# Performance work log

Hardware: AMD Instinct MI355X
Metric: run time of the kernel (lower is better)

## Reference

```python
import jax, jax.numpy as jnp
import numpy as np
import math

# ----- sizes -----
NUM_EDGES = 16384
NUM_NODES = 1024          # senders index into [0, NUM_NODES)
N_MUL = 64                # multiplicity n = V.shape[1]
AVG_NEIGH = 16.0          # avg_num_neighbors
F_IN = 64                 # scalar feature dim of x

# ----- real spherical harmonics (component normalization: sum_m Y_lm^2 = 2l+1) -----
_S3 = math.sqrt(3.0); _S5 = math.sqrt(5.0); _S15 = math.sqrt(15.0)
_C33 = math.sqrt(70.0)/4.0; _C32 = math.sqrt(105.0)/2.0
_C31 = math.sqrt(42.0)/4.0; _C30 = math.sqrt(7.0)/2.0; _CXYZ = math.sqrt(105.0)

def _sph(vn):
    x, y, z = vn[:, 0], vn[:, 1], vn[:, 2]
    Y0 = jnp.ones_like(x)[:, None]
    Y1 = _S3 * vn
    Y2 = jnp.stack([_S15*x*y, _S15*y*z, 0.5*_S5*(3*z*z - 1), _S15*x*z, 0.5*_S15*(x*x - y*y)], axis=1)
    Y3 = jnp.stack([_C33*y*(3*x*x - y*y), _CXYZ*x*y*z, _C31*y*(5*z*z - 1), _C30*z*(5*z*z - 3), _C31*x*(5*z*z - 1), _C32*z*(x*x - y*y), _C33*x*(x*x - 3*y*y)], axis=1)
    return [Y0, Y1, Y2, Y3]

# monomial form of the same SH, used to derive EXACT Clebsch-Gordan coefficients
_SHP = {
    0: [[(1.0, (0,0,0))]],
    1: [[(_S3, (1,0,0))], [(_S3, (0,1,0))], [(_S3, (0,0,1))]],
    2: [[(_S15, (1,1,0))], [(_S15, (0,1,1))], [(1.5*_S5, (0,0,2)), (-0.5*_S5, (0,0,0))], [(_S15, (1,0,1))], [(0.5*_S15, (2,0,0)), (-0.5*_S15, (0,2,0))]],
    3: [[(3*_C33, (2,1,0)), (-_C33, (0,3,0))], [(_CXYZ, (1,1,1))], [(5*_C31, (0,1,2)), (-_C31, (0,1,0))], [(5*_C30, (0,0,3)), (-3*_C30, (0,0,1))], [(5*_C31, (1,0,2)), (-_C31, (1,0,0))], [(_C32, (2,0,1)), (-_C32, (0,2,1))], [(_C33, (3,0,0)), (-3*_C33, (1,2,0))]],
}

def _dfact(n):
    r = 1
    while n > 1:
        r *= n; n -= 2
    return r

def _mono_int(e):
    # exact integral of x^a y^b z^c over the unit sphere
    a, b, c = e
    if (a % 2) or (b % 2) or (c % 2):
        return 0.0
    return 4.0*math.pi*_dfact(a-1)*_dfact(b-1)*_dfact(c-1)/_dfact(a+b+c+1)

def _pmul(p, q):
    return [(cp*cq, (a1+a2, b1+b2, c1+c2)) for cp, (a1,b1,c1) in p for cq, (a2,b2,c2) in q]

def _pint(p):
    return sum(c*_mono_int(e) for c, e in p)

def _cg(l1, l2, l3):
    # unique SO(3) intertwiner in this real-SH basis, scaled like e3nn component norm: sqrt(2l3+1)*w3j
    C = np.zeros((2*l1+1, 2*l2+1, 2*l3+1))
    for i, p1 in enumerate(_SHP[l1]):
        for j, p2 in enumerate(_SHP[l2]):
            p12 = _pmul(p1, p2)
            for k, p3 in enumerate(_SHP[l3]):
                C[i, j, k] = _pint(_pmul(p12, p3)) / (4.0*math.pi)
    return jnp.asarray(C / np.linalg.norm(C) * np.sqrt(2*l3+1), dtype=jnp.float32)

# tensor-product paths surviving filter_ir_out = 0e + 1o + 2e (inputs: SH 0e+1o+2e+3o, V 0e+1o+2e)
_PATHS0 = [(0,0), (1,1), (2,2)]
_PATHS1 = [(0,1), (1,0), (1,2), (2,1), (3,2)]
_PATHS2 = [(0,2), (1,1), (2,0), (2,2), (3,1)]
CGS = {(l1, l2, l3): _cg(l1, l2, l3) for l3, ps in ((0, _PATHS0), (1, _PATHS1), (2, _PATHS2)) for l1, l2 in ps}

# e3nn normalize_function(silu): divide by sqrt(E_{z~N(0,1)}[silu(z)^2])
_zg = np.linspace(-12.0, 12.0, 200001)
_phi = np.exp(-0.5*_zg*_zg)/np.sqrt(2.0*np.pi)
_sl = _zg/(1.0 + np.exp(-_zg))
ACT_C = float(np.sqrt(np.sum(_sl*_sl*_phi)*(_zg[1]-_zg[0])))

def _nsilu(v):
    return jax.nn.silu(v) / ACT_C

def _forward(vectors, x, V, senders, W_w, W1, W2, W3, Wv1, Wv2):
    E, n = V.shape[0], V.shape[1]
    d = jnp.linalg.norm(vectors, axis=1, keepdims=True)                 # [E,1] edge lengths
    vn = vectors / d
    Y = jnp.concatenate(_sph(vn), axis=1)                               # [E,16], ell = 0..3
    w = (x @ W_w) / math.sqrt(x.shape[1])                               # [E,n] edge weights (1-layer MLP, no act)
    wY = w[:, :, None] * Y[:, None, :]                                  # [E,n,16]
    agg = jax.ops.segment_sum(wY, senders, num_segments=NUM_NODES)[senders]  # scatter_sum + map_back
    agg = agg / math.sqrt(AVG_NEIGH)
    A = jnp.split(agg, [1, 4, 9], axis=2)                               # SH chunks: dims 1,3,5,7
    B = jnp.split(V, [1, 4], axis=2)                                    # V chunks: dims 1,3,5
    def tp(l1, l2, l3):
        return jnp.einsum('eni,enj,ijk->enk', A[l1], B[l2], CGS[(l1, l2, l3)])
    scal = jnp.concatenate([tp(a, b, 0) for a, b in _PATHS0], axis=2)   # [E,n,3] new scalars
    V1 = jnp.concatenate([tp(a, b, 1) for a, b in _PATHS1], axis=1)     # [E,5n,3] 1o paths
    V2 = jnp.concatenate([tp(a, b, 2) for a, b in _PATHS2], axis=1)     # [E,5n,5] 2e paths
    h = jnp.concatenate([x, scal.reshape(E, 3*n)], axis=1)              # [E, F_IN+3n]
    h = _nsilu(h @ W1 / math.sqrt(h.shape[1]))
    h = _nsilu(h @ W2 / math.sqrt(W2.shape[0]))
    h = h @ W3 / math.sqrt(W3.shape[0])                                 # output_activation=False
    # poly_envelope(p-1=5, 2), p=6: 1 - 28 d^6 + 48 d^7 - 21 d^8 on [0,1), 0 outside
    u = 1.0 - 28.0*d**6 + 48.0*d**7 - 21.0*d**8
    x_out = jnp.where(d < 1.0, u, 0.0) * h                              # [E,64]
    o1 = jnp.einsum('emi,mo->eoi', V1, Wv1) / math.sqrt(V1.shape[1])    # Linear per irrep: [E,n,3]
    o2 = jnp.einsum('emi,mo->eoi', V2, Wv2) / math.sqrt(V2.shape[1])    # [E,n,5]
    # output 0e block has no input path -> zeros (e3nn Linear, no bias)
    V_out = jnp.concatenate([jnp.zeros((E, n, 1), x_out.dtype), o1, o2], axis=2)  # [E,n,9]
    return x_out, V_out

def setup_inputs():
    key = jax.random.key(0)
    ks = jax.random.split(key, 10)
    E = NUM_EDGES
    vectors = 0.35 * jax.random.normal(ks[0], (E, 3), jnp.float32)   # mostly inside cutoff radius 1
    x = jax.random.normal(ks[1], (E, F_IN), jnp.float32)
    V = jax.random.normal(ks[2], (E, N_MUL, 9), jnp.float32)
    senders = jax.random.randint(ks[3], (E,), 0, NUM_NODES, dtype=jnp.int32)
    W_w = jax.random.normal(ks[4], (F_IN, N_MUL), jnp.float32)
    W1 = jax.random.normal(ks[5], (F_IN + 3*N_MUL, 64), jnp.float32)
    W2 = jax.random.normal(ks[6], (64, 64), jnp.float32)
    W3 = jax.random.normal(ks[7], (64, 64), jnp.float32)
    Wv1 = jax.random.normal(ks[8], (5*N_MUL, N_MUL), jnp.float32)
    Wv2 = jax.random.normal(ks[9], (5*N_MUL, N_MUL), jnp.float32)
    return {"vectors": vectors, "x": x, "V": V, "senders": senders, "W_w": W_w, "W1": W1, "W2": W2, "W3": W3, "Wv1": Wv1, "Wv2": Wv2}

def reference(vectors, x, V, senders, W_w, W1, W2, W3, Wv1, Wv2):
    return _forward(vectors, x, V, senders, W_w, W1, W2, W3, Wv1, Wv2)
```

## Files before the change

kernel.cpp:

```cpp
#include <hip/hip_runtime.h>
#include <math.h>

#define NNODES 1024
#define EB 4

typedef __attribute__((ext_vector_type(8))) short short8;
typedef __attribute__((ext_vector_type(4))) float f32x4;

__device__ __forceinline__ unsigned short f2bf(float f) {
  union { float f; unsigned int u; } v; v.f = f;
  unsigned int r = v.u + 0x7fffu + ((v.u >> 16) & 1u);
  return (unsigned short)(r >> 16);
}

struct CGPack { float v[576]; };

static const double H_SHC[16][2] = {
  {1.0, 0.0},
  {1.7320508075688772, 0.0},
  {1.7320508075688772, 0.0},
  {1.7320508075688772, 0.0},
  {3.8729833462074170, 0.0},
  {3.8729833462074170, 0.0},
  {3.3541019662496844, -1.1180339887498949},
  {3.8729833462074170, 0.0},
  {1.9364916731037085, -1.9364916731037085},
  {6.2749501990055667, -2.0916500663351889},
  {10.246950765959598, 0.0},
  {8.1009258730098255, -1.6201851746019651},
  {6.6143782776614768, -3.9686269665968861},
  {8.1009258730098255, -1.6201851746019651},
  {5.1234753829797990, -5.1234753829797990},
  {2.0916500663351889, -6.2749501990055667},
};
static const int H_SHE[16][2] = {
  {0,0},{1,0},{16,0},{256,0},
  {17,0},{272,0},{512,0},{257,0},{2,32},
  {18,48},{273,0},{528,16},{768,256},{513,1},{258,288},{3,33}};
static const int H_PL1[13] = {0,1,2, 0,1,1,2,3, 0,1,2,2,3};
static const int H_PL2[13] = {0,1,2, 1,0,2,1,2, 2,1,0,2,1};
static const int H_PL3[13] = {0,0,0, 1,1,1,1,1, 2,2,2,2,2};
static const int H_PCG[13] = {0,1,10, 35,44,53,98,143, 248,273,318,343,468};

static double h_dfact(int n) { double r = 1.0; while (n > 1) { r *= n; n -= 2; } return r; }

struct HostConsts {
  CGPack pack;
  float inv_actc;
  HostConsts() {
    const int LOFF[4] = {0,1,4,9};
    for (int p = 0; p < 13; p++) {
      int l1 = H_PL1[p], l2 = H_PL2[p], l3 = H_PL3[p];
      int n1 = 2*l1+1, n2 = 2*l2+1, n3 = 2*l3+1, nent = n1*n2*n3;
      double vals[125], ss = 0.0;
      for (int t = 0; t < nent; t++) {
        int i = t / (n2*n3);
        int rem = t - i*(n2*n3);
        int j = rem / n3;
        int k = rem - j*n3;
        int lm1 = LOFF[l1]+i, lm2 = LOFF[l2]+j, lm3 = LOFF[l3]+k;
        double v = 0.0;
        for (int t1 = 0; t1 < 2; t1++)
        for (int t2 = 0; t2 < 2; t2++)
        for (int t3 = 0; t3 < 2; t3++) {
          double cc = H_SHC[lm1][t1]*H_SHC[lm2][t2]*H_SHC[lm3][t3];
          if (cc == 0.0) continue;
          int s = H_SHE[lm1][t1] + H_SHE[lm2][t2] + H_SHE[lm3][t3];
          int a = s & 15, b = (s >> 4) & 15, c = (s >> 8) & 15;
          if (!((a|b|c) & 1))
            v += cc * (h_dfact(a-1)*h_dfact(b-1)*h_dfact(c-1) / h_dfact(a+b+c+1));
        }
        vals[t] = v; ss += v*v;
      }
      double scale = sqrt((double)(2*l3+1)) / sqrt(ss);
      for (int t = 0; t < nent; t++) pack.v[H_PCG[p]+t] = (float)(vals[t]*scale*0.25);
    }
    pack.v[573] = pack.v[574] = pack.v[575] = 0.f;
    double s = 0.0, dz = 24.0/200000.0;
    for (int i = 0; i <= 200000; i++) {
      double z = -12.0 + dz*i;
      double ph = exp(-0.5*z*z) * 0.39894228040143267794;
      double sl = z / (1.0 + exp(-z));
      s += sl*sl*ph;
    }
    inv_actc = (float)(1.0 / sqrt(s*dz));
  }
};

__global__ __launch_bounds__(256) void k_pre(
    const int* __restrict__ senders, int* __restrict__ counts, int* __restrict__ elist,
    const float* __restrict__ x, const float* __restrict__ Ww,
    float* __restrict__ w_ws,
    const float* __restrict__ Wv1, const float* __restrict__ Wv2,
    const float* __restrict__ W1, const float* __restrict__ W2, const float* __restrict__ W3,
    unsigned short* __restrict__ wv1f, unsigned short* __restrict__ wv2f,
    unsigned short* __restrict__ w1f, unsigned short* __restrict__ w2f,
    unsigned short* __restrict__ w3f,
    float inv_actc, int E)
{
  const int t = threadIdx.x;
  const int bid = blockIdx.x;
  const int nsc = (E + 255) >> 8;

  if (bid < nsc) {
    int e = bid*256 + t;
    if (e < E) {
      int s = senders[e];
      int pos = atomicAdd(&counts[s], 1) & 63;
      elist[s*64 + pos] = e;
    }
    return;
  }

  if (bid < nsc + 32) {
    const int wid = t >> 6, lane = t & 63;
    const int g = (bid - nsc)*4 + wid;
    const float ia = inv_actc;
    const float s320 = 0.05590169943749474f;
    const float* src; unsigned short* dst; int nk, f; float sc;
    if (g < 40)       { src = Wv1; dst = wv1f; nk = 10; f = g;       sc = s320; }
    else if (g < 80)  { src = Wv2; dst = wv2f; nk = 10; f = g - 40;  sc = s320; }
    else if (g < 112) { src = W1;  dst = w1f;  nk = 8;  f = g - 80;  sc = 0.0625f; }
    else if (g < 120) { src = W2;  dst = w2f;  nk = 2;  f = g - 112; sc = 0.125f*ia; }
    else              { src = W3;  dst = w3f;  nk = 2;  f = g - 120; sc = 0.125f*ia; }
    int nt = f / nk;
    int ks = f - nt*nk;
    unsigned short us[8];
    #pragma unroll
    for (int j = 0; j < 8; j++) {
      float v = src[(ks*32 + (lane>>4)*8 + j)*64 + nt*16 + (lane & 15)];
      us[j] = f2bf(v * sc);
    }
    uint4 pk;
    pk.x = (unsigned)us[0] | ((unsigned)us[1] << 16);
    pk.y = (unsigned)us[2] | ((unsigned)us[3] << 16);
    pk.z = (unsigned)us[4] | ((unsigned)us[5] << 16);
    pk.w = (unsigned)us[6] | ((unsigned)us[7] << 16);
    *(uint4*)(dst + ((size_t)f*64 + lane)*8) = pk;
    return;
  }

  __shared__ float xsh[64*64];
  const int eb0 = (bid - nsc - 32) * 64;
  for (int q = t; q < 1024; q += 256)
    ((f32x4*)xsh)[q] = ((const f32x4*)(x + (size_t)eb0*64))[q];

  const int n = t & 63;
  float ww[64];
  #pragma unroll
  for (int f = 0; f < 64; f++) ww[f] = Ww[f*64 + n];
  __syncthreads();

  const int er0 = (t >> 6) * 16;
  #pragma unroll
  for (int i = 0; i < 16; i++) {
    int e = er0 + i;
    const f32x4* xr = (const f32x4*)(&xsh[e*64]);
    float a0 = 0.f, a1 = 0.f, a2 = 0.f, a3 = 0.f;
    #pragma unroll
    for (int fq = 0; fq < 16; fq += 4) {
      f32x4 x0 = xr[fq+0], x1 = xr[fq+1], x2 = xr[fq+2], x3 = xr[fq+3];
      a0 = fmaf(x0.x, ww[fq*4+0],  fmaf(x0.y, ww[fq*4+1],  fmaf(x0.z, ww[fq*4+2],  fmaf(x0.w, ww[fq*4+3],  a0))));
      a1 = fmaf(x1.x, ww[fq*4+4],  fmaf(x1.y, ww[fq*4+5],  fmaf(x1.z, ww[fq*4+6],  fmaf(x1.w, ww[fq*4+7],  a1))));
      a2 = fmaf(x2.x, ww[fq*4+8],  fmaf(x2.y, ww[fq*4+9],  fmaf(x2.z, ww[fq*4+10], fmaf(x2.w, ww[fq*4+11], a2))));
      a3 = fmaf(x3.x, ww[fq*4+12], fmaf(x3.y, ww[fq*4+13], fmaf(x3.z, ww[fq*4+14], fmaf(x3.w, ww[fq*4+15], a3))));
    }
    w_ws[(size_t)(eb0+e)*64 + n] = ((a0+a1)+(a2+a3)) * 0.125f;
  }
}

__global__ __launch_bounds__(256) void k_node(
    const float* __restrict__ vec, const float* __restrict__ w_ws,
    const int* __restrict__ counts, const int* __restrict__ elist,
    float* __restrict__ node_agg)
{
  __shared__ float red[4*1024];
  const int wid = threadIdx.x >> 6, lane = threadIdx.x & 63;
  const int s = blockIdx.x;
  const int deg = min(counts[s], 64);

  const float S3 = 1.7320508075688772f, S5 = 2.23606797749979f, S15 = 3.872983346207417f;
  const float C33 = 2.091650066335189f, C32 = 5.123475382979799f, C31 = 1.6201851746019651f;
  const float C30 = 1.3228756555322954f, CX = 10.246950765959598f;

  float A[16];
  #pragma unroll
  for (int k = 0; k < 16; k++) A[k] = 0.f;

  for (int ii = wid; ii < deg; ii += 4) {
    int e = elist[s*64 + ii];
    float wv = w_ws[(size_t)e*64 + lane];
    float vx = vec[e*3+0], vy = vec[e*3+1], vz = vec[e*3+2];
    float d = sqrtf(vx*vx + vy*vy + vz*vz);
    float X = vx/d, Yv = vy/d, Z = vz/d;
    float y[16];
    y[0] = 1.f;
    y[1] = S3*X;  y[2] = S3*Yv;  y[3] = S3*Z;
    y[4] = S15*X*Yv; y[5] = S15*Yv*Z; y[6] = 0.5f*S5*(3.f*Z*Z - 1.f);
    y[7] = S15*X*Z;  y[8] = 0.5f*S15*(X*X - Yv*Yv);
    y[9]  = C33*Yv*(3.f*X*X - Yv*Yv);
    y[10] = CX*X*Yv*Z;
    y[11] = C31*Yv*(5.f*Z*Z - 1.f);
    y[12] = C30*Z*(5.f*Z*Z - 3.f);
    y[13] = C31*X*(5.f*Z*Z - 1.f);
    y[14] = C32*Z*(X*X - 3.f*Yv*Yv)*0.f + C32*Z*(X*X - Yv*Yv);
    y[14] = C32*Z*(X*X - Yv*Yv);
    y[15] = C33*X*(X*X - 3.f*Yv*Yv);
    #pragma unroll
    for (int k = 0; k < 16; k++) A[k] = fmaf(wv, y[k], A[k]);
  }
  #pragma unroll
  for (int k = 0; k < 16; k++) red[wid*1024 + lane*16 + k] = A[k];
  __syncthreads();
  const int t = threadIdx.x;
  f32x4 v0 = ((f32x4*)red)[t];
  f32x4 v1 = ((f32x4*)red)[256 + t];
  f32x4 v2 = ((f32x4*)red)[512 + t];
  f32x4 v3 = ((f32x4*)red)[768 + t];
  f32x4 sum = v0 + v1 + v2 + v3;
  ((f32x4*)(node_agg + (size_t)s*1024))[t] = sum;
}

template<int L1, int L2, int L3>
__device__ __forceinline__ void tp_path(const float* __restrict__ cgp,
    const float a[16], const float b[9], float o[2*L3+1])
{
  constexpr int N1 = 2*L1+1, N2 = 2*L2+1, N3 = 2*L3+1;
  constexpr int AO = (L1==0) ? 0 : (L1==1) ? 1 : (L1==2) ? 4 : 9;
  constexpr int BO = (L2==0) ? 0 : (L2==1) ? 1 : 4;
  constexpr int LM1 = (L1==0) ? 0 : (L1==1) ? 1 : (L1==2) ? 4 : 9;
  constexpr int LM2 = (L2==0) ? 0 : (L2==1) ? 1 : 4;
  constexpr int LM3 = (L3==0) ? 0 : (L3==1) ? 1 : 4;
  static constexpr unsigned char PAR[16] =
      {0, 1,2,4, 3,6,0,5,0, 2,7,2,4,1,4,1};
  #pragma unroll
  for (int k = 0; k < N3; k++) o[k] = 0.f;
  int ci = 0;
  #pragma unroll
  for (int i = 0; i < N1; i++) {
    #pragma unroll
    for (int j = 0; j < N2; j++) {
      float ab = a[AO+i] * b[BO+j];
      #pragma unroll
      for (int k = 0; k < N3; k++) {
        if ((PAR[LM1+i] ^ PAR[LM2+j] ^ PAR[LM3+k]) == 0)
          o[k] = fmaf(ab, cgp[ci], o[k]);
        ci++;
      }
    }
  }
}

__global__ __launch_bounds__(256, 6) void edge_main(
    const float* __restrict__ vec, const float* __restrict__ x,
    const float* __restrict__ V, const int* __restrict__ senders,
    const float* __restrict__ node_agg, const CGPack P,
    const unsigned short* __restrict__ wv1f, const unsigned short* __restrict__ wv2f,
    const unsigned short* __restrict__ w1f, const unsigned short* __restrict__ w2f,
    const unsigned short* __restrict__ w3f,
    float* __restrict__ out, int E)
{
  __shared__ __align__(16) unsigned short V12sh[32*328];
  __shared__ __align__(16) unsigned short zrow[336];
  __shared__ __align__(16) unsigned short hsh[4*264];
  __shared__ __align__(16) unsigned short h1sh[4*72];
  __shared__ __align__(16) unsigned short h2sh[4*72];
  __shared__ __align__(16) float xosh[4*64];
  __shared__ float ush[EB];

  unsigned short* V1sh = V12sh;
  unsigned short* V2sh = V12sh + 12*328;
  float* vosh = (float*)V12sh;

  const float* cg = P.v;

  const int t = threadIdx.x;
  const int wid = t >> 6, lane = t & 63;
  const int e0 = blockIdx.x * EB;
  const size_t E64 = (size_t)E * 64;

  if (t < 168) ((unsigned int*)zrow)[t] = 0u;

  if (t < 64) {
    int el = t >> 4, off = (t & 15)*4;
    f32x4 xv = *(const f32x4*)(x + (size_t)(e0 + el)*64 + off);
    uint2 pk;
    pk.x = (unsigned)f2bf(xv.x) | ((unsigned)f2bf(xv.y) << 16);
    pk.y = (unsigned)f2bf(xv.z) | ((unsigned)f2bf(xv.w) << 16);
    *(uint2*)(hsh + el*264 + off) = pk;
  }

  {
    const int eloc = wid;
    const int eg = e0 + eloc;

    float b[9];
    const float* vp = V + (size_t)eg*576 + lane*9;
    #pragma unroll
    for (int j = 0; j < 9; j++) b[j] = vp[j];

    const int s = senders[eg];
    float a[16];
    const f32x4* nap = (const f32x4*)(node_agg + s*1024 + lane*16);
    #pragma unroll
    for (int q = 0; q < 4; q++) {
      f32x4 av = nap[q];
      a[q*4+0] = av.x; a[q*4+1] = av.y; a[q*4+2] = av.z; a[q*4+3] = av.w;
    }

    float o1[1], o3[3], o5[5];
    tp_path<0,0,0>(cg + 0,  a, b, o1); hsh[eloc*264 + 64 + lane*3 + 0] = f2bf(o1[0]);
    tp_path<1,1,0>(cg + 1,  a, b, o1); hsh[eloc*264 + 64 + lane*3 + 1] = f2bf(o1[0]);
    tp_path<2,2,0>(cg + 10, a, b, o1); hsh[eloc*264 + 64 + lane*3 + 2] = f2bf(o1[0]);
    tp_path<0,1,1>(cg + 35, a, b, o3);
    { int r = eloc*3; for (int i=0;i<3;i++) V1sh[(r+i)*328 + 0*64 + lane] = f2bf(o3[i]); }
    tp_path<1,0,1>(cg + 44, a, b, o3);
    { int r = eloc*3; for (int i=0;i<3;i++) V1sh[(r+i)*328 + 1*64 + lane] = f2bf(o3[i]); }
    tp_path<1,2,1>(cg + 53, a, b, o3);
    { int r = eloc*3; for (int i=0;i<3;i++) V1sh[(r+i)*328 + 2*64 + lane] = f2bf(o3[i]); }
    tp_path<2,1,1>(cg + 98, a, b, o3);
    { int r = eloc*3; for (int i=0;i<3;i++) V1sh[(r+i)*328 + 3*64 + lane] = f2bf(o3[i]); }
    tp_path<3,2,1>(cg + 143, a, b, o3);
    { int r = eloc*3; for (int i=0;i<3;i++) V1sh[(r+i)*328 + 4*64 + lane] = f2bf(o3[i]); }
    tp_path<0,2,2>(cg + 248, a, b, o5);
    { int r = eloc*5; for (int i=0;i<5;i++) V2sh[(r+i)*328 + 0*64 + lane] = f2bf(o5[i]); }
    tp_path<1,1,2>(cg + 273, a, b, o5);
    { int r = eloc*5; for (int i=0;i<5;i++) V2sh[(r+i)*328 + 1*64 + lane] = f2bf(o5[i]); }
    tp_path<2,0,2>(cg + 318, a, b, o5);
    { int r = eloc*5; for (int i=0;i<5;i++) V2sh[(r+i)*328 + 2*64 + lane] = f2bf(o5[i]); }
    tp_path<2,2,2>(cg + 343, a, b, o5);
    { int r = eloc*5; for (int i=0;i<5;i++) V2sh[(r+i)*328 + 3*64 + lane] = f2bf(o5[i]); }
    tp_path<3,1,2>(cg + 468, a, b, o5);
    { int r = eloc*5; for (int i=0;i<5;i++) V2sh[(r+i)*328 + 4*64 + lane] = f2bf(o5[i]); }

    if (lane == 0) {
      float vx = vec[eg*3+0], vy = vec[eg*3+1], vz = vec[eg*3+2];
      float d = sqrtf(vx*vx + vy*vy + vz*vz);
      float u = 0.f;
      if (d < 1.f) {
        float d3 = d*d*d, d6 = d3*d3, d7 = d6*d, d8 = d7*d;
        u = 1.f - 28.f*d6 + 48.f*d7 - 21.f*d8;
      }
      ush[eloc] = u;
    }
  }
  __syncthreads();

  const int ntile = wid;
  const int qr = lane >> 4;
  const int ml = lane & 15;

  f32x4 acc1 = (f32x4){0,0,0,0};
  {
    const unsigned short* p0 = (ml < 12) ? &V1sh[ml*328] : zrow;
    const unsigned short* bb = wv1f + ((size_t)(ntile*10)*64 + lane)*8;
    #pragma unroll
    for (int ks = 0; ks < 10; ks++) {
      short8 bf = *(const short8*)(bb + ks*512);
      short8 af = *(const short8*)(p0 + ks*32 + qr*8);
      acc1 = __builtin_amdgcn_mfma_f32_16x16x32_bf16(af, bf, acc1, 0, 0, 0);
    }
  }

  f32x4 acc2a = (f32x4){0,0,0,0}, acc2b = (f32x4){0,0,0,0};
  {
    const unsigned short* p0 = &V2sh[ml*328];
    const unsigned short* p1 = (16+ml < 20) ? &V2sh[(16+ml)*328] : zrow;
    const unsigned short* bb = wv2f + ((size_t)(ntile*10)*64 + lane)*8;
    #pragma unroll
    for (int ks = 0; ks < 10; ks++) {
      short8 bf = *(const short8*)(bb + ks*512);
      int ao = ks*32 + qr*8;
      short8 af0 = *(const short8*)(p0 + ao);
      short8 af1 = *(const short8*)(p1 + ao);
      acc2a = __builtin_amdgcn_mfma_f32_16x16x32_bf16(af0, bf, acc2a, 0, 0, 0);
      acc2b = __builtin_amdgcn_mfma_f32_16x16x32_bf16(af1, bf, acc2b, 0, 0, 0);
    }
  }

  const unsigned short* hp = (ml < 4) ? &hsh[ml*264] : zrow;
  {
    f32x4 c = (f32x4){0,0,0,0};
    const unsigned short* bb = w1f + ((size_t)(ntile*8)*64 + lane)*8;
    #pragma unroll
    for (int ks = 0; ks < 8; ks++) {
      short8 bf = *(const short8*)(bb + ks*512);
      short8 af = *(const short8*)(hp + ks*32 + qr*8);
      c = __builtin_amdgcn_mfma_f32_16x16x32_bf16(af, bf, c, 0, 0, 0);
    }
    #pragma unroll
    for (int r = 0; r < 4; r++) {
      int row = qr*4 + r;
      if (row < 4) {
        float v = c[r];
        float sv = v / (1.f + expf(-v));
        h1sh[row*72 + ntile*16 + ml] = f2bf(sv);
      }
    }
  }
  __syncthreads();

  #pragma unroll
  for (int r = 0; r < 4; r++) {
    int row = qr*4 + r;
    if (row < 12) {
      int el = row / 3, i = row - (row/3)*3;
      vosh[el*584 + (ntile*16+ml)*9 + 1 + i] = acc1[r];
    }
  }
  #pragma unroll
  for (int r = 0; r < 4; r++) {
    int row = qr*4 + r;
    int el = row / 5, i = row - (row/5)*5;
    vosh[el*584 + (ntile*16+ml)*9 + 4 + i] = acc2a[r];
  }
  #pragma unroll
  for (int r = 0; r < 4; r++) {
    int row = 16 + qr*4 + r;
    if (row < 20) {
      int el = row / 5, i = row - (row/5)*5;
      vosh[el*584 + (ntile*16+ml)*9 + 4 + i] = acc2b[r];
    }
  }
  { int el = t >> 6, o = t & 63;
    vosh[el*584 + o*9] = 0.f; }

  {
    f32x4 c = (f32x4){0,0,0,0};
    const unsigned short* ap = (ml < 4) ? &h1sh[ml*72] : zrow;
    const unsigned short* bb = w2f + ((size_t)(ntile*2)*64 + lane)*8;
    #pragma unroll
    for (int ks = 0; ks < 2; ks++) {
      short8 bf = *(const short8*)(bb + ks*512);
      short8 af = *(const short8*)(ap + ks*32 + qr*8);
      c = __builtin_amdgcn_mfma_f32_16x16x32_bf16(af, bf, c, 0, 0, 0);
    }
    #pragma unroll
    for (int r = 0; r < 4; r++) {
      int row = qr*4 + r;
      if (row < 4) {
        float v = c[r];
        float sv = v / (1.f + expf(-v));
        h2sh[row*72 + ntile*16 + ml] = f2bf(sv);
      }
    }
  }
  __syncthreads();

  {
    f32x4 c = (f32x4){0,0,0,0};
    const unsigned short* ap = (ml < 4) ? &h2sh[ml*72] : zrow;
    const unsigned short* bb = w3f + ((size_t)(ntile*2)*64 + lane)*8;
    #pragma unroll
    for (int ks = 0; ks < 2; ks++) {
      short8 bf = *(const short8*)(bb + ks*512);
      short8 af = *(const short8*)(ap + ks*32 + qr*8);
      c = __builtin_amdgcn_mfma_f32_16x16x32_bf16(af, bf, c, 0, 0, 0);
    }
    #pragma unroll
    for (int r = 0; r < 4; r++) {
      int row = qr*4 + r;
      if (row < 4) xosh[row*64 + ntile*16 + ml] = ush[row] * c[r];
    }
  }

  for (int q = t; q < 576; q += 256) {
    int el = q / 144, i4 = q - (q/144)*144;
    ((f32x4*)(out + E64 + (size_t)(e0+el)*576))[i4] = ((f32x4*)(vosh + el*584))[i4];
  }
  __syncthreads();

  if (t < 64)
    ((f32x4*)(out + (size_t)e0*64))[t] = ((f32x4*)xosh)[t];
}

extern "C" void kernel_launch(void* const* d_in, const int* in_sizes, int n_in,
                              void* d_out, int out_size, void* d_ws, size_t ws_size,
                              hipStream_t stream)
{
  const float* vec     = (const float*)d_in[0];
  const float* x       = (const float*)d_in[1];
  const float* V       = (const float*)d_in[2];
  const int*   senders = (const int*)  d_in[3];
  const float* Ww      = (const float*)d_in[4];
  const float* W1      = (const float*)d_in[5];
  const float* W2      = (const float*)d_in[6];
  const float* W3      = (const float*)d_in[7];
  const float* Wv1     = (const float*)d_in[8];
  const float* Wv2     = (const float*)d_in[9];
  float* out = (float*)d_out;
  const int E = in_sizes[0] / 3;

  static HostConsts HC;

  char* base = (char*)d_ws;
  float* node_agg = (float*)(base);
  float* w_ws     = (float*)(base + (4<<20));
  int* counts     = (int*)  (base + (8<<20) + 8192);
  int* elist      = (int*)  (base + (8<<20) + 12288);
  unsigned short* wv1f = (unsigned short*)(base + (8<<20) + 278528);
  unsigned short* wv2f = (unsigned short*)(base + (8<<20) + 319488);
  unsigned short* w1f  = (unsigned short*)(base + (8<<20) + 360448);
  unsigned short* w2f  = (unsigned short*)(base + (8<<20) + 393216);
  unsigned short* w3f  = (unsigned short*)(base + (8<<20) + 401408);

  hipMemsetAsync(counts, 0, NNODES*sizeof(int), stream);

  const int nsc = (E + 255) >> 8;
  const int ngemm = (E + 63) >> 6;
  k_pre<<<nsc + 32 + ngemm, 256, 0, stream>>>(senders, counts, elist,
                                      x, Ww, w_ws,
                                      Wv1, Wv2, W1, W2, W3,
                                      wv1f, wv2f, w1f, w2f, w3f, HC.inv_actc, E);
  k_node<<<NNODES, 256, 0, stream>>>(vec, w_ws, counts, elist, node_agg);
  edge_main<<<E/EB, 256, 0, stream>>>(vec, x, V, senders, node_agg, HC.pack,
                                      wv1f, wv2f, w1f, w2f, w3f, out, E);
}
```

Measured before the change: 165.9 us.

## Fuse three kernels into one persistent kernel with software grid barriers

```diff
diff --git a/kernel.cpp b/kernel.cpp
--- a/kernel.cpp
+++ b/kernel.cpp
@@ -3,6 +3,7 @@
 
 #define NNODES 1024
 #define EB 4
+#define GRID 1024
 
 typedef __attribute__((ext_vector_type(8))) short short8;
 typedef __attribute__((ext_vector_type(4))) float f32x4;
@@ -87,140 +88,6 @@
   }
 };
 
-__global__ __launch_bounds__(256) void k_pre(
-    const int* __restrict__ senders, int* __restrict__ counts, int* __restrict__ elist,
-    const float* __restrict__ x, const float* __restrict__ Ww,
-    float* __restrict__ w_ws,
-    const float* __restrict__ Wv1, const float* __restrict__ Wv2,
-    const float* __restrict__ W1, const float* __restrict__ W2, const float* __restrict__ W3,
-    unsigned short* __restrict__ wv1f, unsigned short* __restrict__ wv2f,
-    unsigned short* __restrict__ w1f, unsigned short* __restrict__ w2f,
-    unsigned short* __restrict__ w3f,
-    float inv_actc, int E)
-{
-  const int t = threadIdx.x;
-  const int bid = blockIdx.x;
-  const int nsc = (E + 255) >> 8;
-
-  if (bid < nsc) {
-    int e = bid*256 + t;
-    if (e < E) {
-      int s = senders[e];
-      int pos = atomicAdd(&counts[s], 1) & 63;
-      elist[s*64 + pos] = e;
-    }
-    return;
-  }
-
-  if (bid < nsc + 32) {
-    const int wid = t >> 6, lane = t & 63;
-    const int g = (bid - nsc)*4 + wid;
-    const float ia = inv_actc;
-    const float s320 = 0.05590169943749474f;
-    const float* src; unsigned short* dst; int nk, f; float sc;
-    if (g < 40)       { src = Wv1; dst = wv1f; nk = 10; f = g;       sc = s320; }
-    else if (g < 80)  { src = Wv2; dst = wv2f; nk = 10; f = g - 40;  sc = s320; }
-    else if (g < 112) { src = W1;  dst = w1f;  nk = 8;  f = g - 80;  sc = 0.0625f; }
-    else if (g < 120) { src = W2;  dst = w2f;  nk = 2;  f = g - 112; sc = 0.125f*ia; }
-    else              { src = W3;  dst = w3f;  nk = 2;  f = g - 120; sc = 0.125f*ia; }
-    int nt = f / nk;
-    int ks = f - nt*nk;
-    unsigned short us[8];
-    #pragma unroll
-    for (int j = 0; j < 8; j++) {
-      float v = src[(ks*32 + (lane>>4)*8 + j)*64 + nt*16 + (lane & 15)];
-      us[j] = f2bf(v * sc);
-    }
-    uint4 pk;
-    pk.x = (unsigned)us[0] | ((unsigned)us[1] << 16);
-    pk.y = (unsigned)us[2] | ((unsigned)us[3] << 16);
-    pk.z = (unsigned)us[4] | ((unsigned)us[5] << 16);
-    pk.w = (unsigned)us[6] | ((unsigned)us[7] << 16);
-    *(uint4*)(dst + ((size_t)f*64 + lane)*8) = pk;
-    return;
-  }
-
-  __shared__ float xsh[64*64];
-  const int eb0 = (bid - nsc - 32) * 64;
-  for (int q = t; q < 1024; q += 256)
-    ((f32x4*)xsh)[q] = ((const f32x4*)(x + (size_t)eb0*64))[q];
-
-  const int n = t & 63;
-  float ww[64];
-  #pragma unroll
-  for (int f = 0; f < 64; f++) ww[f] = Ww[f*64 + n];
-  __syncthreads();
-
-  const int er0 = (t >> 6) * 16;
-  #pragma unroll
-  for (int i = 0; i < 16; i++) {
-    int e = er0 + i;
-    const f32x4* xr = (const f32x4*)(&xsh[e*64]);
-    float a0 = 0.f, a1 = 0.f, a2 = 0.f, a3 = 0.f;
-    #pragma unroll
-    for (int fq = 0; fq < 16; fq += 4) {
-      f32x4 x0 = xr[fq+0], x1 = xr[fq+1], x2 = xr[fq+2], x3 = xr[fq+3];
-      a0 = fmaf(x0.x, ww[fq*4+0],  fmaf(x0.y, ww[fq*4+1],  fmaf(x0.z, ww[fq*4+2],  fmaf(x0.w, ww[fq*4+3],  a0))));
-      a1 = fmaf(x1.x, ww[fq*4+4],  fmaf(x1.y, ww[fq*4+5],  fmaf(x1.z, ww[fq*4+6],  fmaf(x1.w, ww[fq*4+7],  a1))));
-      a2 = fmaf(x2.x, ww[fq*4+8],  fmaf(x2.y, ww[fq*4+9],  fmaf(x2.z, ww[fq*4+10], fmaf(x2.w, ww[fq*4+11], a2))));
-      a3 = fmaf(x3.x, ww[fq*4+12], fmaf(x3.y, ww[fq*4+13], fmaf(x3.z, ww[fq*4+14], fmaf(x3.w, ww[fq*4+15], a3))));
-    }
-    w_ws[(size_t)(eb0+e)*64 + n] = ((a0+a1)+(a2+a3)) * 0.125f;
-  }
-}
-
-__global__ __launch_bounds__(256) void k_node(
-    const float* __restrict__ vec, const float* __restrict__ w_ws,
-    const int* __restrict__ counts, const int* __restrict__ elist,
-    float* __restrict__ node_agg)
-{
-  __shared__ float red[4*1024];
-  const int wid = threadIdx.x >> 6, lane = threadIdx.x & 63;
-  const int s = blockIdx.x;
-  const int deg = min(counts[s], 64);
-
-  const float S3 = 1.7320508075688772f, S5 = 2.23606797749979f, S15 = 3.872983346207417f;
-  const float C33 = 2.091650066335189f, C32 = 5.123475382979799f, C31 = 1.6201851746019651f;
-  const float C30 = 1.3228756555322954f, CX = 10.246950765959598f;
-
-  float A[16];
-  #pragma unroll
-  for (int k = 0; k < 16; k++) A[k] = 0.f;
-
-  for (int ii = wid; ii < deg; ii += 4) {
-    int e = elist[s*64 + ii];
-    float wv = w_ws[(size_t)e*64 + lane];
-    float vx = vec[e*3+0], vy = vec[e*3+1], vz = vec[e*3+2];
-    float d = sqrtf(vx*vx + vy*vy + vz*vz);
-    float X = vx/d, Yv = vy/d, Z = vz/d;
-    float y[16];
-    y[0] = 1.f;
-    y[1] = S3*X;  y[2] = S3*Yv;  y[3] = S3*Z;
-    y[4] = S15*X*Yv; y[5] = S15*Yv*Z; y[6] = 0.5f*S5*(3.f*Z*Z - 1.f);
-    y[7] = S15*X*Z;  y[8] = 0.5f*S15*(X*X - Yv*Yv);
-    y[9]  = C33*Yv*(3.f*X*X - Yv*Yv);
-    y[10] = CX*X*Yv*Z;
-    y[11] = C31*Yv*(5.f*Z*Z - 1.f);
-    y[12] = C30*Z*(5.f*Z*Z - 3.f);
-    y[13] = C31*X*(5.f*Z*Z - 1.f);
-    y[14] = C32*Z*(X*X - 3.f*Yv*Yv)*0.f + C32*Z*(X*X - Yv*Yv);
-    y[14] = C32*Z*(X*X - Yv*Yv);
-    y[15] = C33*X*(X*X - 3.f*Yv*Yv);
-    #pragma unroll
-    for (int k = 0; k < 16; k++) A[k] = fmaf(wv, y[k], A[k]);
-  }
-  #pragma unroll
-  for (int k = 0; k < 16; k++) red[wid*1024 + lane*16 + k] = A[k];
-  __syncthreads();
-  const int t = threadIdx.x;
-  f32x4 v0 = ((f32x4*)red)[t];
-  f32x4 v1 = ((f32x4*)red)[256 + t];
-  f32x4 v2 = ((f32x4*)red)[512 + t];
-  f32x4 v3 = ((f32x4*)red)[768 + t];
-  f32x4 sum = v0 + v1 + v2 + v3;
-  ((f32x4*)(node_agg + (size_t)s*1024))[t] = sum;
-}
-
 template<int L1, int L2, int L3>
 __device__ __forceinline__ void tp_path(const float* __restrict__ cgp,
     const float a[16], const float b[9], float o[2*L3+1])
@@ -251,13 +118,30 @@
   }
 }
 
-__global__ __launch_bounds__(256, 6) void edge_main(
+__device__ __forceinline__ void grid_bar(int* ctr, int nblk) {
+  __syncthreads();
+  if (threadIdx.x == 0) {
+    __threadfence();
+    __hip_atomic_fetch_add(ctr, 1, __ATOMIC_RELEASE, __HIP_MEMORY_SCOPE_AGENT);
+    while (__hip_atomic_load(ctr, __ATOMIC_ACQUIRE, __HIP_MEMORY_SCOPE_AGENT) < nblk)
+      __builtin_amdgcn_s_sleep(2);
+    __threadfence();
+  }
+  __syncthreads();
+}
+
+__global__ __launch_bounds__(256, 4) void mega(
     const float* __restrict__ vec, const float* __restrict__ x,
     const float* __restrict__ V, const int* __restrict__ senders,
-    const float* __restrict__ node_agg, const CGPack P,
-    const unsigned short* __restrict__ wv1f, const unsigned short* __restrict__ wv2f,
-    const unsigned short* __restrict__ w1f, const unsigned short* __restrict__ w2f,
-    const unsigned short* __restrict__ w3f,
+    const float* __restrict__ Ww,
+    const float* __restrict__ Wv1, const float* __restrict__ Wv2,
+    const float* __restrict__ W1, const float* __restrict__ W2, const float* __restrict__ W3,
+    const CGPack P, float inv_actc,
+    float* __restrict__ node_agg, float* __restrict__ w_ws,
+    int* __restrict__ counts, int* __restrict__ elist, int* __restrict__ bars,
+    unsigned short* __restrict__ wv1f, unsigned short* __restrict__ wv2f,
+    unsigned short* __restrict__ w1f, unsigned short* __restrict__ w2f,
+    unsigned short* __restrict__ w3f,
     float* __restrict__ out, int E)
 {
   __shared__ __align__(16) unsigned short V12sh[32*328];
@@ -268,210 +152,323 @@
   __shared__ __align__(16) float xosh[4*64];
   __shared__ float ush[EB];
 
+  const int t = threadIdx.x;
+  const int bid = blockIdx.x;
+  const int wid = t >> 6, lane = t & 63;
+  const int nblk = gridDim.x;
+
+  if (bid < 256) {
+    float* xsh = (float*)V12sh;
+    const int eb0 = bid * 64;
+    for (int q = t; q < 1024; q += 256)
+      ((f32x4*)xsh)[q] = ((const f32x4*)(x + (size_t)eb0*64))[q];
+    const int n = t & 63;
+    float ww[64];
+    #pragma unroll
+    for (int f = 0; f < 64; f++) ww[f] = Ww[f*64 + n];
+    __syncthreads();
+    const int er0 = (t >> 6) * 16;
+    #pragma unroll
+    for (int i = 0; i < 16; i++) {
+      int e = er0 + i;
+      const f32x4* xr = (const f32x4*)(&xsh[e*64]);
+      float a0 = 0.f, a1 = 0.f, a2 = 0.f, a3 = 0.f;
+      #pragma unroll
+      for (int fq = 0; fq < 16; fq += 4) {
+        f32x4 x0 = xr[fq+0], x1 = xr[fq+1], x2 = xr[fq+2], x3 = xr[fq+3];
+        a0 = fmaf(x0.x, ww[fq*4+0],  fmaf(x0.y, ww[fq*4+1],  fmaf(x0.z, ww[fq*4+2],  fmaf(x0.w, ww[fq*4+3],  a0))));
+        a1 = fmaf(x1.x, ww[fq*4+4],  fmaf(x1.y, ww[fq*4+5],  fmaf(x1.z, ww[fq*4+6],  fmaf(x1.w, ww[fq*4+7],  a1))));
+        a2 = fmaf(x2.x, ww[fq*4+8],  fmaf(x2.y, ww[fq*4+9],  fmaf(x2.z, ww[fq*4+10], fmaf(x2.w, ww[fq*4+11], a2))));
+        a3 = fmaf(x3.x, ww[fq*4+12], fmaf(x3.y, ww[fq*4+13], fmaf(x3.z, ww[fq*4+14], fmaf(x3.w, ww[fq*4+15], a3))));
+      }
+      w_ws[(size_t)(eb0+e)*64 + n] = ((a0+a1)+(a2+a3)) * 0.125f;
+    }
+  } else if (bid < 288) {
+    const int g = (bid - 256)*4 + wid;
+    const float ia = inv_actc;
+    const float s320 = 0.05590169943749474f;
+    const float* src; unsigned short* dst; int nk, f; float sc;
+    if (g < 40)       { src = Wv1; dst = wv1f; nk = 10; f = g;       sc = s320; }
+    else if (g < 80)  { src = Wv2; dst = wv2f; nk = 10; f = g - 40;  sc = s320; }
+    else if (g < 112) { src = W1;  dst = w1f;  nk = 8;  f = g - 80;  sc = 0.0625f; }
+    else if (g < 120) { src = W2;  dst = w2f;  nk = 2;  f = g - 112; sc = 0.125f*ia; }
+    else              { src = W3;  dst = w3f;  nk = 2;  f = g - 120; sc = 0.125f*ia; }
+    int nt = f / nk;
+    int ks = f - nt*nk;
+    unsigned short us[8];
+    #pragma unroll
+    for (int j = 0; j < 8; j++) {
+      float v = src[(ks*32 + (lane>>4)*8 + j)*64 + nt*16 + (lane & 15)];
+      us[j] = f2bf(v * sc);
+    }
+    uint4 pk;
+    pk.x = (unsigned)us[0] | ((unsigned)us[1] << 16);
+    pk.y = (unsigned)us[2] | ((unsigned)us[3] << 16);
+    pk.z = (unsigned)us[4] | ((unsigned)us[5] << 16);
+    pk.w = (unsigned)us[6] | ((unsigned)us[7] << 16);
+    *(uint4*)(dst + ((size_t)f*64 + lane)*8) = pk;
+  } else if (bid < 352) {
+    int e = (bid - 288)*256 + t;
+    if (e < E) {
+      int s = senders[e];
+      int pos = atomicAdd(&counts[s], 1) & 63;
+      elist[s*64 + pos] = e;
+    }
+  }
+
+  grid_bar(&bars[0], nblk);
+
+  {
+    float* red = (float*)V12sh;
+    const int s = bid;
+    const int deg = min(counts[s], 64);
+
+    const float S3 = 1.7320508075688772f, S5 = 2.23606797749979f, S15 = 3.872983346207417f;
+    const float C33 = 2.091650066335189f, C32 = 5.123475382979799f, C31 = 1.6201851746019651f;
+    const float C30 = 1.3228756555322954f, CX = 10.246950765959598f;
+
+    float A[16];
+    #pragma unroll
+    for (int k = 0; k < 16; k++) A[k] = 0.f;
+
+    for (int ii = wid; ii < deg; ii += 4) {
+      int e = elist[s*64 + ii];
+      float wv = w_ws[(size_t)e*64 + lane];
+      float vx = vec[e*3+0], vy = vec[e*3+1], vz = vec[e*3+2];
+      float d = sqrtf(vx*vx + vy*vy + vz*vz);
+      float X = vx/d, Yv = vy/d, Z = vz/d;
+      float y[16];
+      y[0] = 1.f;
+      y[1] = S3*X;  y[2] = S3*Yv;  y[3] = S3*Z;
+      y[4] = S15*X*Yv; y[5] = S15*Yv*Z; y[6] = 0.5f*S5*(3.f*Z*Z - 1.f);
+      y[7] = S15*X*Z;  y[8] = 0.5f*S15*(X*X - Yv*Yv);
+      y[9]  = C33*Yv*(3.f*X*X - Yv*Yv);
+      y[10] = CX*X*Yv*Z;
+      y[11] = C31*Yv*(5.f*Z*Z - 1.f);
+      y[12] = C30*Z*(5.f*Z*Z - 3.f);
+      y[13] = C31*X*(5.f*Z*Z - 1.f);
+      y[14] = C32*Z*(X*X - Yv*Yv);
+      y[15] = C33*X*(X*X - 3.f*Yv*Yv);
+      #pragma unroll
+      for (int k = 0; k < 16; k++) A[k] = fmaf(wv, y[k], A[k]);
+    }
+    #pragma unroll
+    for (int k = 0; k < 16; k++) red[wid*1024 + lane*16 + k] = A[k];
+    __syncthreads();
+    f32x4 v0 = ((f32x4*)red)[t];
+    f32x4 v1 = ((f32x4*)red)[256 + t];
+    f32x4 v2 = ((f32x4*)red)[512 + t];
+    f32x4 v3 = ((f32x4*)red)[768 + t];
+    f32x4 sum = v0 + v1 + v2 + v3;
+    ((f32x4*)(node_agg + (size_t)s*1024))[t] = sum;
+  }
+
+  grid_bar(&bars[1], nblk);
+
   unsigned short* V1sh = V12sh;
   unsigned short* V2sh = V12sh + 12*328;
   float* vosh = (float*)V12sh;
-
   const float* cg = P.v;
-
-  const int t = threadIdx.x;
-  const int wid = t >> 6, lane = t & 63;
-  const int e0 = blockIdx.x * EB;
   const size_t E64 = (size_t)E * 64;
-
-  if (t < 168) ((unsigned int*)zrow)[t] = 0u;
-
-  if (t < 64) {
-    int el = t >> 4, off = (t & 15)*4;
-    f32x4 xv = *(const f32x4*)(x + (size_t)(e0 + el)*64 + off);
-    uint2 pk;
-    pk.x = (unsigned)f2bf(xv.x) | ((unsigned)f2bf(xv.y) << 16);
-    pk.y = (unsigned)f2bf(xv.z) | ((unsigned)f2bf(xv.w) << 16);
-    *(uint2*)(hsh + el*264 + off) = pk;
-  }
-
-  {
-    const int eloc = wid;
-    const int eg = e0 + eloc;
-
-    float b[9];
-    const float* vp = V + (size_t)eg*576 + lane*9;
-    #pragma unroll
-    for (int j = 0; j < 9; j++) b[j] = vp[j];
-
-    const int s = senders[eg];
-    float a[16];
-    const f32x4* nap = (const f32x4*)(node_agg + s*1024 + lane*16);
-    #pragma unroll
-    for (int q = 0; q < 4; q++) {
-      f32x4 av = nap[q];
-      a[q*4+0] = av.x; a[q*4+1] = av.y; a[q*4+2] = av.z; a[q*4+3] = av.w;
-    }
-
-    float o1[1], o3[3], o5[5];
-    tp_path<0,0,0>(cg + 0,  a, b, o1); hsh[eloc*264 + 64 + lane*3 + 0] = f2bf(o1[0]);
-    tp_path<1,1,0>(cg + 1,  a, b, o1); hsh[eloc*264 + 64 + lane*3 + 1] = f2bf(o1[0]);
-    tp_path<2,2,0>(cg + 10, a, b, o1); hsh[eloc*264 + 64 + lane*3 + 2] = f2bf(o1[0]);
-    tp_path<0,1,1>(cg + 35, a, b, o3);
-    { int r = eloc*3; for (int i=0;i<3;i++) V1sh[(r+i)*328 + 0*64 + lane] = f2bf(o3[i]); }
-    tp_path<1,0,1>(cg + 44, a, b, o3);
-    { int r = eloc*3; for (int i=0;i<3;i++) V1sh[(r+i)*328 + 1*64 + lane] = f2bf(o3[i]); }
-    tp_path<1,2,1>(cg + 53, a, b, o3);
-    { int r = eloc*3; for (int i=0;i<3;i++) V1sh[(r+i)*328 + 2*64 + lane] = f2bf(o3[i]); }
-    tp_path<2,1,1>(cg + 98, a, b, o3);
-    { int r = eloc*3; for (int i=0;i<3;i++) V1sh[(r+i)*328 + 3*64 + lane] = f2bf(o3[i]); }
-    tp_path<3,2,1>(cg + 143, a, b, o3);
-    { int r = eloc*3; for (int i=0;i<3;i++) V1sh[(r+i)*328 + 4*64 + lane] = f2bf(o3[i]); }
-    tp_path<0,2,2>(cg + 248, a, b, o5);
-    { int r = eloc*5; for (int i=0;i<5;i++) V2sh[(r+i)*328 + 0*64 + lane] = f2bf(o5[i]); }
-    tp_path<1,1,2>(cg + 273, a, b, o5);
-    { int r = eloc*5; for (int i=0;i<5;i++) V2sh[(r+i)*328 + 1*64 + lane] = f2bf(o5[i]); }
-    tp_path<2,0,2>(cg + 318, a, b, o5);
-    { int r = eloc*5; for (int i=0;i<5;i++) V2sh[(r+i)*328 + 2*64 + lane] = f2bf(o5[i]); }
-    tp_path<2,2,2>(cg + 343, a, b, o5);
-    { int r = eloc*5; for (int i=0;i<5;i++) V2sh[(r+i)*328 + 3*64 + lane] = f2bf(o5[i]); }
-    tp_path<3,1,2>(cg + 468, a, b, o5);
-    { int r = eloc*5; for (int i=0;i<5;i++) V2sh[(r+i)*328 + 4*64 + lane] = f2bf(o5[i]); }
-
-    if (lane == 0) {
-      float vx = vec[eg*3+0], vy = vec[eg*3+1], vz = vec[eg*3+2];
-      float d = sqrtf(vx*vx + vy*vy + vz*vz);
-      float u = 0.f;
-      if (d < 1.f) {
-        float d3 = d*d*d, d6 = d3*d3, d7 = d6*d, d8 = d7*d;
-        u = 1.f - 28.f*d6 + 48.f*d7 - 21.f*d8;
-      }
-      ush[eloc] = u;
-    }
-  }
-  __syncthreads();
-
   const int ntile = wid;
   const int qr = lane >> 4;
   const int ml = lane & 15;
 
-  f32x4 acc1 = (f32x4){0,0,0,0};
-  {
-    const unsigned short* p0 = (ml < 12) ? &V1sh[ml*328] : zrow;
-    const unsigned short* bb = wv1f + ((size_t)(ntile*10)*64 + lane)*8;
-    #pragma unroll
-    for (int ks = 0; ks < 10; ks++) {
-      short8 bf = *(const short8*)(bb + ks*512);
-      short8 af = *(const short8*)(p0 + ks*32 + qr*8);
-      acc1 = __builtin_amdgcn_mfma_f32_16x16x32_bf16(af, bf, acc1, 0, 0, 0);
-    }
-  }
-
-  f32x4 acc2a = (f32x4){0,0,0,0}, acc2b = (f32x4){0,0,0,0};
-  {
-    const unsigned short* p0 = &V2sh[ml*328];
-    const unsigned short* p1 = (16+ml < 20) ? &V2sh[(16+ml)*328] : zrow;
-    const unsigned short* bb = wv2f + ((size_t)(ntile*10)*64 + lane)*8;
-    #pragma unroll
-    for (int ks = 0; ks < 10; ks++) {
-      short8 bf = *(const short8*)(bb + ks*512);
-      int ao = ks*32 + qr*8;
-      short8 af0 = *(const short8*)(p0 + ao);
-      short8 af1 = *(const short8*)(p1 + ao);
-      acc2a = __builtin_amdgcn_mfma_f32_16x16x32_bf16(af0, bf, acc2a, 0, 0, 0);
-      acc2b = __builtin_amdgcn_mfma_f32_16x16x32_bf16(af1, bf, acc2b, 0, 0, 0);
-    }
-  }
-
-  const unsigned short* hp = (ml < 4) ? &hsh[ml*264] : zrow;
-  {
-    f32x4 c = (f32x4){0,0,0,0};
-    const unsigned short* bb = w1f + ((size_t)(ntile*8)*64 + lane)*8;
-    #pragma unroll
-    for (int ks = 0; ks < 8; ks++) {
-      short8 bf = *(const short8*)(bb + ks*512);
-      short8 af = *(const short8*)(hp + ks*32 + qr*8);
-      c = __builtin_amdgcn_mfma_f32_16x16x32_bf16(af, bf, c, 0, 0, 0);
-    }
+  if (t < 168) ((unsigned int*)zrow)[t] = 0u;
+
+  for (int it = 0; it < 4; ++it) {
+    const int e0 = bid*16 + it*4;
+
+    if (t < 64) {
+      int el = t >> 4, off = (t & 15)*4;
+      f32x4 xv = *(const f32x4*)(x + (size_t)(e0 + el)*64 + off);
+      uint2 pk;
+      pk.x = (unsigned)f2bf(xv.x) | ((unsigned)f2bf(xv.y) << 16);
+      pk.y = (unsigned)f2bf(xv.z) | ((unsigned)f2bf(xv.w) << 16);
+      *(uint2*)(hsh + el*264 + off) = pk;
+    }
+
+    {
+      const int eloc = wid;
+      const int eg = e0 + eloc;
+
+      float b[9];
+      const float* vp = V + (size_t)eg*576 + lane*9;
+      #pragma unroll
+      for (int j = 0; j < 9; j++) b[j] = vp[j];
+
+      const int s = senders[eg];
+      float a[16];
+      const f32x4* nap = (const f32x4*)(node_agg + s*1024 + lane*16);
+      #pragma unroll
+      for (int q = 0; q < 4; q++) {
+        f32x4 av = nap[q];
+        a[q*4+0] = av.x; a[q*4+1] = av.y; a[q*4+2] = av.z; a[q*4+3] = av.w;
+      }
+
+      float o1[1], o3[3], o5[5];
+      tp_path<0,0,0>(cg + 0,  a, b, o1); hsh[eloc*264 + 64 + lane*3 + 0] = f2bf(o1[0]);
+      tp_path<1,1,0>(cg + 1,  a, b, o1); hsh[eloc*264 + 64 + lane*3 + 1] = f2bf(o1[0]);
+      tp_path<2,2,0>(cg + 10, a, b, o1); hsh[eloc*264 + 64 + lane*3 + 2] = f2bf(o1[0]);
+      tp_path<0,1,1>(cg + 35, a, b, o3);
+      { int r = eloc*3; for (int i=0;i<3;i++) V1sh[(r+i)*328 + 0*64 + lane] = f2bf(o3[i]); }
+      tp_path<1,0,1>(cg + 44, a, b, o3);
+      { int r = eloc*3; for (int i=0;i<3;i++) V1sh[(r+i)*328 + 1*64 + lane] = f2bf(o3[i]); }
+      tp_path<1,2,1>(cg + 53, a, b, o3);
+      { int r = eloc*3; for (int i=0;i<3;i++) V1sh[(r+i)*328 + 2*64 + lane] = f2bf(o3[i]); }
+      tp_path<2,1,1>(cg + 98, a, b, o3);
+      { int r = eloc*3; for (int i=0;i<3;i++) V1sh[(r+i)*328 + 3*64 + lane] = f2bf(o3[i]); }
+      tp_path<3,2,1>(cg + 143, a, b, o3);
+      { int r = eloc*3; for (int i=0;i<3;i++) V1sh[(r+i)*328 + 4*64 + lane] = f2bf(o3[i]); }
+      tp_path<0,2,2>(cg + 248, a, b, o5);
+      { int r = eloc*5; for (int i=0;i<5;i++) V2sh[(r+i)*328 + 0*64 + lane] = f2bf(o5[i]); }
+      tp_path<1,1,2>(cg + 273, a, b, o5);
+      { int r = eloc*5; for (int i=0;i<5;i++) V2sh[(r+i)*328 + 1*64 + lane] = f2bf(o5[i]); }
+      tp_path<2,0,2>(cg + 318, a, b, o5);
+      { int r = eloc*5; for (int i=0;i<5;i++) V2sh[(r+i)*328 + 2*64 + lane] = f2bf(o5[i]); }
+      tp_path<2,2,2>(cg + 343, a, b, o5);
+      { int r = eloc*5; for (int i=0;i<5;i++) V2sh[(r+i)*328 + 3*64 + lane] = f2bf(o5[i]); }
+      tp_path<3,1,2>(cg + 468, a, b, o5);
+      { int r = eloc*5; for (int i=0;i<5;i++) V2sh[(r+i)*328 + 4*64 + lane] = f2bf(o5[i]); }
+
+      if (lane == 0) {
+        float vx = vec[eg*3+0], vy = vec[eg*3+1], vz = vec[eg*3+2];
+        float d = sqrtf(vx*vx + vy*vy + vz*vz);
+        float u = 0.f;
+        if (d < 1.f) {
+          float d3 = d*d*d, d6 = d3*d3, d7 = d6*d, d8 = d7*d;
+          u = 1.f - 28.f*d6 + 48.f*d7 - 21.f*d8;
+        }
+        ush[eloc] = u;
+      }
+    }
+    __syncthreads();
+
+    f32x4 acc1 = (f32x4){0,0,0,0};
+    {
+      const unsigned short* p0 = (ml < 12) ? &V1sh[ml*328] : zrow;
+      const unsigned short* bb = wv1f + ((size_t)(ntile*10)*64 + lane)*8;
+      #pragma unroll
+      for (int ks = 0; ks < 10; ks++) {
+        short8 bf = *(const short8*)(bb + ks*512);
+        short8 af = *(const short8*)(p0 + ks*32 + qr*8);
+        acc1 = __builtin_amdgcn_mfma_f32_16x16x32_bf16(af, bf, acc1, 0, 0, 0);
+      }
+    }
+
+    f32x4 acc2a = (f32x4){0,0,0,0}, acc2b = (f32x4){0,0,0,0};
+    {
+      const unsigned short* p0 = &V2sh[ml*328];
+      const unsigned short* p1 = (16+ml < 20) ? &V2sh[(16+ml)*328] : zrow;
+      const unsigned short* bb = wv2f + ((size_t)(ntile*10)*64 + lane)*8;
+      #pragma unroll
+      for (int ks = 0; ks < 10; ks++) {
+        short8 bf = *(const short8*)(bb + ks*512);
+        int ao = ks*32 + qr*8;
+        short8 af0 = *(const short8*)(p0 + ao);
+        short8 af1 = *(const short8*)(p1 + ao);
+        acc2a = __builtin_amdgcn_mfma_f32_16x16x32_bf16(af0, bf, acc2a, 0, 0, 0);
+        acc2b = __builtin_amdgcn_mfma_f32_16x16x32_bf16(af1, bf, acc2b, 0, 0, 0);
+      }
+    }
+
+    {
+      f32x4 c = (f32x4){0,0,0,0};
+      const unsigned short* hp = (ml < 4) ? &hsh[ml*264] : zrow;
+      const unsigned short* bb = w1f + ((size_t)(ntile*8)*64 + lane)*8;
+      #pragma unroll
+      for (int ks = 0; ks < 8; ks++) {
+        short8 bf = *(const short8*)(bb + ks*512);
+        short8 af = *(const short8*)(hp + ks*32 + qr*8);
+        c = __builtin_amdgcn_mfma_f32_16x16x32_bf16(af, bf, c, 0, 0, 0);
+      }
+      #pragma unroll
+      for (int r = 0; r < 4; r++) {
+        int row = qr*4 + r;
+        if (row < 4) {
+          float v = c[r];
+          float sv = v / (1.f + expf(-v));
+          h1sh[row*72 + ntile*16 + ml] = f2bf(sv);
+        }
+      }
+    }
+    __syncthreads();
+
     #pragma unroll
     for (int r = 0; r < 4; r++) {
       int row = qr*4 + r;
-      if (row < 4) {
-        float v = c[r];
-        float sv = v / (1.f + expf(-v));
-        h1sh[row*72 + ntile*16 + ml] = f2bf(sv);
-      }
-    }
-  }
-  __syncthreads();
-
-  #pragma unroll
-  for (int r = 0; r < 4; r++) {
-    int row = qr*4 + r;
-    if (row < 12) {
-      int el = row / 3, i = row - (row/3)*3;
-      vosh[el*584 + (ntile*16+ml)*9 + 1 + i] = acc1[r];
-    }
-  }
-  #pragma unroll
-  for (int r = 0; r < 4; r++) {
-    int row = qr*4 + r;
-    int el = row / 5, i = row - (row/5)*5;
-    vosh[el*584 + (ntile*16+ml)*9 + 4 + i] = acc2a[r];
-  }
-  #pragma unroll
-  for (int r = 0; r < 4; r++) {
-    int row = 16 + qr*4 + r;
-    if (row < 20) {
-      int el = row / 5, i = row - (row/5)*5;
-      vosh[el*584 + (ntile*16+ml)*9 + 4 + i] = acc2b[r];
-    }
-  }
-  { int el = t >> 6, o = t & 63;
-    vosh[el*584 + o*9] = 0.f; }
-
-  {
-    f32x4 c = (f32x4){0,0,0,0};
-    const unsigned short* ap = (ml < 4) ? &h1sh[ml*72] : zrow;
-    const unsigned short* bb = w2f + ((size_t)(ntile*2)*64 + lane)*8;
-    #pragma unroll
-    for (int ks = 0; ks < 2; ks++) {
-      short8 bf = *(const short8*)(bb + ks*512);
-      short8 af = *(const short8*)(ap + ks*32 + qr*8);
-      c = __builtin_amdgcn_mfma_f32_16x16x32_bf16(af, bf, c, 0, 0, 0);
+      if (row < 12) {
+        int el = row / 3, i = row - (row/3)*3;
+        vosh[el*584 + (ntile*16+ml)*9 + 1 + i] = acc1[r];
+      }
     }
     #pragma unroll
     for (int r = 0; r < 4; r++) {
       int row = qr*4 + r;
-      if (row < 4) {
-        float v = c[r];
-        float sv = v / (1.f + expf(-v));
-        h2sh[row*72 + ntile*16 + ml] = f2bf(sv);
-      }
-    }
+      int el = row / 5, i = row - (row/5)*5;
+      vosh[el*584 + (ntile*16+ml)*9 + 4 + i] = acc2a[r];
+    }
+    #pragma unroll
+    for (int r = 0; r < 4; r++) {
+      int row = 16 + qr*4 + r;
+      if (row < 20) {
+        int el = row / 5, i = row - (row/5)*5;
+        vosh[el*584 + (ntile*16+ml)*9 + 4 + i] = acc2b[r];
+      }
+    }
+    { int el = t >> 6, o = t & 63;
+      vosh[el*584 + o*9] = 0.f; }
+
+    {
+      f32x4 c = (f32x4){0,0,0,0};
+      const unsigned short* ap = (ml < 4) ? &h1sh[ml*72] : zrow;
+      const unsigned short* bb = w2f + ((size_t)(ntile*2)*64 + lane)*8;
+      #pragma unroll
+      for (int ks = 0; ks < 2; ks++) {
+        short8 bf = *(const short8*)(bb + ks*512);
+        short8 af = *(const short8*)(ap + ks*32 + qr*8);
+        c = __builtin_amdgcn_mfma_f32_16x16x32_bf16(af, bf, c, 0, 0, 0);
+      }
+      #pragma unroll
+      for (int r = 0; r < 4; r++) {
+        int row = qr*4 + r;
+        if (row < 4) {
+          float v = c[r];
+          float sv = v / (1.f + expf(-v));
+          h2sh[row*72 + ntile*16 + ml] = f2bf(sv);
+        }
+      }
+    }
+    __syncthreads();
+
+    {
+      f32x4 c = (f32x4){0,0,0,0};
+      const unsigned short* ap = (ml < 4) ? &h2sh[ml*72] : zrow;
+      const unsigned short* bb = w3f + ((size_t)(ntile*2)*64 + lane)*8;
+      #pragma unroll
+      for (int ks = 0; ks < 2; ks++) {
+        short8 bf = *(const short8*)(bb + ks*512);
+        short8 af = *(const short8*)(ap + ks*32 + qr*8);
+        c = __builtin_amdgcn_mfma_f32_16x16x32_bf16(af, bf, c, 0, 0, 0);
+      }
+      #pragma unroll
+      for (int r = 0; r < 4; r++) {
+        int row = qr*4 + r;
+        if (row < 4) xosh[row*64 + ntile*16 + ml] = ush[row] * c[r];
+      }
+    }
+
+    for (int q = t; q < 576; q += 256) {
+      int el = q / 144, i4 = q - (q/144)*144;
+      ((f32x4*)(out + E64 + (size_t)(e0+el)*576))[i4] = ((f32x4*)(vosh + el*584))[i4];
+    }
+    __syncthreads();
+
+    if (t < 64)
+      ((f32x4*)(out + (size_t)e0*64))[t] = ((f32x4*)xosh)[t];
+
+    __syncthreads();
   }
-  __syncthreads();
-
-  {
-    f32x4 c = (f32x4){0,0,0,0};
-    const unsigned short* ap = (ml < 4) ? &h2sh[ml*72] : zrow;
-    const unsigned short* bb = w3f + ((size_t)(ntile*2)*64 + lane)*8;
-    #pragma unroll
-    for (int ks = 0; ks < 2; ks++) {
-      short8 bf = *(const short8*)(bb + ks*512);
-      short8 af = *(const short8*)(ap + ks*32 + qr*8);
-      c = __builtin_amdgcn_mfma_f32_16x16x32_bf16(af, bf, c, 0, 0, 0);
-    }
-    #pragma unroll
-    for (int r = 0; r < 4; r++) {
-      int row = qr*4 + r;
-      if (row < 4) xosh[row*64 + ntile*16 + ml] = ush[row] * c[r];
-    }
-  }
-
-  for (int q = t; q < 576; q += 256) {
-    int el = q / 144, i4 = q - (q/144)*144;
-    ((f32x4*)(out + E64 + (size_t)(e0+el)*576))[i4] = ((f32x4*)(vosh + el*584))[i4];
-  }
-  __syncthreads();
-
-  if (t < 64)
-    ((f32x4*)(out + (size_t)e0*64))[t] = ((f32x4*)xosh)[t];
 }
 
 extern "C" void kernel_launch(void* const* d_in, const int* in_sizes, int n_in,
@@ -497,22 +494,19 @@
   float* node_agg = (float*)(base);
   float* w_ws     = (float*)(base + (4<<20));
   int* counts     = (int*)  (base + (8<<20) + 8192);
-  int* elist      = (int*)  (base + (8<<20) + 12288);
+  int* bars       = (int*)  (base + (8<<20) + 12288);
+  int* elist      = (int*)  (base + (8<<20) + 16384);
   unsigned short* wv1f = (unsigned short*)(base + (8<<20) + 278528);
   unsigned short* wv2f = (unsigned short*)(base + (8<<20) + 319488);
   unsigned short* w1f  = (unsigned short*)(base + (8<<20) + 360448);
   unsigned short* w2f  = (unsigned short*)(base + (8<<20) + 393216);
   unsigned short* w3f  = (unsigned short*)(base + (8<<20) + 401408);
 
-  hipMemsetAsync(counts, 0, NNODES*sizeof(int), stream);
-
-  const int nsc = (E + 255) >> 8;
-  const int ngemm = (E + 63) >> 6;
-  k_pre<<<nsc + 32 + ngemm, 256, 0, stream>>>(senders, counts, elist,
-                                      x, Ww, w_ws,
-                                      Wv1, Wv2, W1, W2, W3,
-                                      wv1f, wv2f, w1f, w2f, w3f, HC.inv_actc, E);
-  k_node<<<NNODES, 256, 0, stream>>>(vec, w_ws, counts, elist, node_agg);
-  edge_main<<<E/EB, 256, 0, stream>>>(vec, x, V, senders, node_agg, HC.pack,
-                                      wv1f, wv2f, w1f, w2f, w3f, out, E);
+  hipMemsetAsync(counts, 0, 4096 + 128, stream);
+
+  mega<<<GRID, 256, 0, stream>>>(vec, x, V, senders, Ww,
+                                 Wv1, Wv2, W1, W2, W3,
+                                 HC.pack, HC.inv_actc,
+                                 node_agg, w_ws, counts, elist, bars,
+                                 wv1f, wv2f, w1f, w2f, w3f, out, E);
 }
```

After: 502.2 us. 3.03x slower.
